# Kernel optimization log

Hardware: AMD Instinct MI355X
Metric: run time of the kernel (lower is better)

The kernel has to match this reference:

```python
import jax, jax.numpy as jnp
import numpy as np

K = 3  # number of propagation hops in SGConv


def setup_inputs() -> dict:
    key = jax.random.key(0)
    k1, k2, k3, k4 = jax.random.split(key, 4)
    N, E, F_in, F_out = 100000, 1600000, 32, 64
    x = jax.random.normal(k1, (N, F_in), dtype=jnp.float32)
    edge_index = jax.random.randint(k2, (2, E), 0, N, dtype=jnp.int64)
    # Linear(in_channels, hidden_channels) params, torch layout: W [out, in], b [out]
    lim = 1.0 / np.sqrt(F_in)
    W = jax.random.uniform(k3, (F_out, F_in), minval=-lim, maxval=lim, dtype=jnp.float32)
    b = jax.random.uniform(k4, (F_out,), minval=-lim, maxval=lim, dtype=jnp.float32)
    return {"x": x, "edge_index": edge_index, "W": W, "b": b}


def reference(x, edge_index, W, b):
    N = x.shape[0]
    # gcn_norm: add self-loops with weight 1, symmetric normalization
    loop = jnp.arange(N, dtype=edge_index.dtype)
    src = jnp.concatenate([edge_index[0], loop])  # [E+N] message sources (x_j)
    dst = jnp.concatenate([edge_index[1], loop])  # [E+N] aggregation targets
    ones = jnp.ones(src.shape[0], dtype=x.dtype)
    deg = jax.ops.segment_sum(ones, dst, num_segments=N)  # in-degree incl. self-loop
    dinv = jnp.where(deg > 0, jax.lax.rsqrt(deg), 0.0)
    norm = dinv[src] * dinv[dst]  # [E+N]
    # K hops of normalized sparse propagation: x <- \hat{A} x
    h = x
    for _ in range(K):
        h = jax.ops.segment_sum(norm[:, None] * h[src], dst, num_segments=N)
    # final linear transform
    return h @ W.T + b
```

## Files before the change

kernel.cpp:

```cpp
#include <hip/hip_runtime.h>


#define F_IN 32
#define F_OUT 64
#define SB_SHIFT 13
#define MAXSB 16
#define SUB_SHIFT 9
#define SUB (1 << SUB_SHIFT)
#define EPB1 2048
#define EPB2 4096
#define SCAP 147456
#define SUBCAP 12288
#define BPS (SCAP / EPB2)

typedef float f4 __attribute__((ext_vector_type(4)));
typedef _Float16 h4 __attribute__((ext_vector_type(4)));
typedef int i2 __attribute__((ext_vector_type(2)));

__global__ __launch_bounds__(256) void k_bin1(const int* __restrict__ ei,
                                              int* __restrict__ scur,
                                              unsigned* __restrict__ b1, int E) {
    __shared__ unsigned stage[EPB1];
    __shared__ unsigned char bidl[EPB1];
    __shared__ int hist[MAXSB], lscan[MAXSB], lbase[MAXSB], fcur[MAXSB];
    unsigned rec[EPB1 / 256];
    int      bk[EPB1 / 256];
    int tid = threadIdx.x;
    int base = blockIdx.x * EPB1;
    int cnt = E - base; if (cnt > EPB1) cnt = EPB1;

    if (tid < MAXSB) hist[tid] = 0;
    __syncthreads();
#pragma unroll
    for (int k = 0; k < EPB1 / 256; ++k) {
        int i = base + k * 256 + tid;
        bk[k] = -1;
        if (i < E) {
            unsigned s = (unsigned)ei[i];
            unsigned d = (unsigned)ei[E + i];
            int b = d >> SB_SHIFT;
            rec[k] = (s << SB_SHIFT) | (d & ((1u << SB_SHIFT) - 1));
            bk[k] = b;
            atomicAdd(&hist[b], 1);
        }
    }
    __syncthreads();
    if (tid < 64) {
        int c = (tid < MAXSB) ? hist[tid] : 0;
        int inc = c;
#pragma unroll
        for (int off = 1; off < MAXSB; off <<= 1) {
            int t = __shfl_up(inc, off);
            if (tid >= off) inc += t;
        }
        if (tid < MAXSB) {
            lscan[tid] = inc - c;
            fcur[tid] = inc - c;
            lbase[tid] = c ? atomicAdd(&scur[tid], c) : 0;
        }
    }
    __syncthreads();
#pragma unroll
    for (int k = 0; k < EPB1 / 256; ++k) {
        if (bk[k] >= 0) {
            int loc = atomicAdd(&fcur[bk[k]], 1);
            stage[loc] = rec[k];
            bidl[loc] = (unsigned char)bk[k];
        }
    }
    __syncthreads();
    for (int k = 0; k < EPB1 / 256; ++k) {
        int idx = k * 256 + tid;
        if (idx < cnt) {
            int b = bidl[idx];
            b1[(size_t)b * SCAP + lbase[b] + (idx - lscan[b])] = stage[idx];
        }
    }
}

__global__ __launch_bounds__(256) void k_bin2(const unsigned* __restrict__ b1,
                                              const int* __restrict__ scur,
                                              int* __restrict__ subcur,
                                              unsigned* __restrict__ b2) {
    int sb = blockIdx.x / BPS;
    int base = (blockIdx.x % BPS) * EPB2;
    int count = scur[sb];
    if (base >= count) return;
    int cnt = count - base; if (cnt > EPB2) cnt = EPB2;
    const unsigned* src = b1 + (size_t)sb * SCAP + base;

    __shared__ unsigned stage[EPB2];
    __shared__ int hist[16], lscan[16], lbase[16], fcur[16];
    unsigned rec[EPB2 / 256];
    int tid = threadIdx.x;
    if (tid < 16) hist[tid] = 0;
    __syncthreads();
#pragma unroll
    for (int k = 0; k < EPB2 / 256; ++k) {
        int i = k * 256 + tid;
        rec[k] = 0xFFFFFFFFu;
        if (i < cnt) {
            unsigned r = src[i];
            rec[k] = r;
            atomicAdd(&hist[(r >> SUB_SHIFT) & 15], 1);
        }
    }
    __syncthreads();
    if (tid < 64) {
        int c = (tid < 16) ? hist[tid] : 0;
        int inc = c;
#pragma unroll
        for (int off = 1; off < 16; off <<= 1) {
            int t = __shfl_up(inc, off);
            if (tid >= off) inc += t;
        }
        if (tid < 16) {
            lscan[tid] = inc - c;
            fcur[tid] = inc - c;
            lbase[tid] = c ? atomicAdd(&subcur[sb * 16 + tid], c) : 0;
        }
    }
    __syncthreads();
#pragma unroll
    for (int k = 0; k < EPB2 / 256; ++k) {
        if (rec[k] != 0xFFFFFFFFu) {
            int b = (rec[k] >> SUB_SHIFT) & 15;
            int loc = atomicAdd(&fcur[b], 1);
            stage[loc] = rec[k];
        }
    }
    __syncthreads();
    for (int k = 0; k < EPB2 / 256; ++k) {
        int idx = k * 256 + tid;
        if (idx < cnt) {
            unsigned r = stage[idx];
            int b = (r >> SUB_SHIFT) & 15;
            unsigned packed = ((r >> SB_SHIFT) << SUB_SHIFT) | (r & (SUB - 1));
            b2[(size_t)(sb * 16 + b) * SUBCAP + lbase[b] + (idx - lscan[b])] = packed;
        }
    }
}

__global__ __launch_bounds__(512) void k_fill3(const unsigned* __restrict__ b2,
                                               const int* __restrict__ subcur,
                                               float* __restrict__ dinv,
                                               i2* __restrict__ rp2,
                                               int* __restrict__ col, int N) {
    __shared__ unsigned stage[SUBCAP];
    __shared__ int h[SUB];
    __shared__ int wsum[8];
    int tid = threadIdx.x;
    int g = blockIdx.x;
    int count = subcur[g];
    int sbase = g * SUBCAP;

    h[tid] = 0;
    for (int e = tid; e < count; e += 512) stage[e] = b2[(size_t)sbase + e];
    __syncthreads();
    for (int e = tid; e < count; e += 512) atomicAdd(&h[stage[e] & (SUB - 1)], 1);
    __syncthreads();

    int deg = h[tid];
    int lane = tid & 63, wid = tid >> 6;
    int inc = deg;
#pragma unroll
    for (int off = 1; off < 64; off <<= 1) {
        int t = __shfl_up(inc, off);
        if (lane >= off) inc += t;
    }
    if (lane == 63) wsum[wid] = inc;
    __syncthreads();
    if (wid == 0) {
        int v = (lane < 8) ? wsum[lane] : 0;
#pragma unroll
        for (int off = 1; off < 8; off <<= 1) {
            int t = __shfl_up(v, off);
            if (lane >= off) v += t;
        }
        if (lane < 8) wsum[lane] = v;
    }
    __syncthreads();
    int incl = inc + (wid ? wsum[wid - 1] : 0);
    int excl = incl - deg;

    int node = (g << SUB_SHIFT) + tid;
    if (node < N) {
        dinv[node] = rsqrtf(1.0f + (float)deg);
        rp2[node] = (i2){sbase + excl, sbase + incl};
    }
    h[tid] = excl;
    __syncthreads();

    for (int e = tid; e < count; e += 512) {
        unsigned r = stage[e];
        int slot = sbase + atomicAdd(&h[r & (SUB - 1)], 1);
        col[slot] = (int)(r >> SUB_SHIFT);
    }
}

__global__ void k_prescale(const f4* __restrict__ x, const float* __restrict__ dinv,
                           h4* __restrict__ g, int N8) {
    int t = blockIdx.x * blockDim.x + threadIdx.x;
    if (t < N8) {
        f4 v = dinv[t >> 3] * x[t];
        g[t] = __builtin_convertvector(v, h4);
    }
}

__global__ __launch_bounds__(256) void k_hop_gather(const i2* __restrict__ rp2,
                                                    const int* __restrict__ col,
                                                    const float* __restrict__ dinv,
                                                    const h4* __restrict__ gin,
                                                    h4* __restrict__ gout, int N) {
    int t = blockIdx.x * blockDim.x + threadIdx.x;
    int n = t >> 3;
    if (n >= N) return;
    int q = t & 7;
    i2 r2 = rp2[n];
    int e0 = r2.x, e1 = r2.y;
    f4 a0 = __builtin_convertvector(gin[n * 8 + q], f4);
    f4 a1 = {0.f, 0.f, 0.f, 0.f};
    int e = e0;
    for (; e + 3 < e1; e += 4) {
        int s0 = col[e], s1 = col[e + 1], s2 = col[e + 2], s3 = col[e + 3];
        h4 h0 = gin[s0 * 8 + q];
        h4 h1 = gin[s1 * 8 + q];
        h4 h2 = gin[s2 * 8 + q];
        h4 h3 = gin[s3 * 8 + q];
        a0 += __builtin_convertvector(h0, f4);
        a1 += __builtin_convertvector(h1, f4);
        a0 += __builtin_convertvector(h2, f4);
        a1 += __builtin_convertvector(h3, f4);
    }
    for (; e < e1; ++e) a0 += __builtin_convertvector(gin[col[e] * 8 + q], f4);
    float di = dinv[n];
    float sc = di * di;
    f4 r = sc * (a0 + a1);
    gout[n * 8 + q] = __builtin_convertvector(r, h4);
}

__global__ __launch_bounds__(256) void k_hop3_linear(const i2* __restrict__ rp2,
                                                     const int* __restrict__ col,
                                                     const float* __restrict__ dinv,
                                                     const h4* __restrict__ gin,
                                                     const float* __restrict__ W,
                                                     const float* __restrict__ bias,
                                                     float* __restrict__ out, int N) {
    __shared__ float Wl[F_OUT][F_IN + 1];
    __shared__ float hl[32][F_IN + 1];
    int tid = threadIdx.x;
    for (int idx = tid; idx < F_OUT * F_IN; idx += 256)
        Wl[idx >> 5][idx & 31] = W[idx];

    int nl = tid >> 3;
    int q = tid & 7;
    int n = blockIdx.x * 32 + nl;
    if (n < N) {
        i2 r2 = rp2[n];
        int e0 = r2.x, e1 = r2.y;
        f4 a0 = __builtin_convertvector(gin[n * 8 + q], f4);
        f4 a1 = {0.f, 0.f, 0.f, 0.f};
        int e = e0;
        for (; e + 3 < e1; e += 4) {
            int s0 = col[e], s1 = col[e + 1], s2 = col[e + 2], s3 = col[e + 3];
            h4 h0 = gin[s0 * 8 + q];
            h4 h1 = gin[s1 * 8 + q];
            h4 h2 = gin[s2 * 8 + q];
            h4 h3 = gin[s3 * 8 + q];
            a0 += __builtin_convertvector(h0, f4);
            a1 += __builtin_convertvector(h1, f4);
            a0 += __builtin_convertvector(h2, f4);
            a1 += __builtin_convertvector(h3, f4);
        }
        for (; e < e1; ++e) a0 += __builtin_convertvector(gin[col[e] * 8 + q], f4);
        float di = dinv[n];
        f4 r = di * (a0 + a1);
        hl[nl][q * 4 + 0] = r.x;
        hl[nl][q * 4 + 1] = r.y;
        hl[nl][q * 4 + 2] = r.z;
        hl[nl][q * 4 + 3] = r.w;
    }
    __syncthreads();
    int obase = q * 8;
    if (n < N) {
        float acc[8];
#pragma unroll
        for (int j = 0; j < 8; ++j) acc[j] = bias[obase + j];
#pragma unroll
        for (int f = 0; f < F_IN; ++f) {
            float hv = hl[nl][f];
#pragma unroll
            for (int j = 0; j < 8; ++j) acc[j] += hv * Wl[obase + j][f];
        }
        float* op = out + (size_t)n * F_OUT + obase;
        f4 v0 = {acc[0], acc[1], acc[2], acc[3]};
        f4 v1 = {acc[4], acc[5], acc[6], acc[7]};
        *(f4*)op = v0;
        *(f4*)(op + 4) = v1;
    }
}

extern "C" void kernel_launch(void* const* d_in, const int* in_sizes, int n_in,
                              void* d_out, int out_size, void* d_ws, size_t ws_size,
                              hipStream_t stream) {
    const float* x  = (const float*)d_in[0];
    const int*   ei = (const int*)d_in[1];
    const float* W  = (const float*)d_in[2];
    const float* b  = (const float*)d_in[3];
    float* out = (float*)d_out;

    const int N = in_sizes[0] / F_IN;
    const int E = in_sizes[1] / 2;
    const int NSUB = (N + SUB - 1) >> SUB_SHIFT;

    int* scur   = (int*)d_ws;
    int* subcur = scur + MAXSB;
    i2*  rp2    = (i2*)(subcur + MAXSB * 16);
    float* dinv = (float*)(rp2 + N);
    unsigned* b1 = (unsigned*)(((uintptr_t)(dinv + N) + 255) & ~(uintptr_t)255);
    unsigned* b2 = b1 + (size_t)MAXSB * SCAP;
    int* col     = (int*)(b2 + (size_t)MAXSB * 16 * SUBCAP);
    _Float16* hA = (_Float16*)(((uintptr_t)(col + (size_t)MAXSB * 16 * SUBCAP) + 255)
                               & ~(uintptr_t)255);
    _Float16* hB  = hA + (size_t)N * F_IN;
    _Float16* hB2 = hB + (size_t)N * F_IN;

    const int B = 256;
    dim3 blk(B);

    hipMemsetAsync(scur, 0, (MAXSB + MAXSB * 16) * sizeof(int), stream);

    k_bin1<<<dim3((E + EPB1 - 1) / EPB1), blk, 0, stream>>>(ei, scur, b1, E);
    k_bin2<<<dim3(((N + (1 << SB_SHIFT) - 1) >> SB_SHIFT) * BPS), blk, 0, stream>>>(
        b1, scur, subcur, b2);

    k_fill3<<<dim3(NSUB), dim3(512), 0, stream>>>(b2, subcur, dinv, rp2, col, N);

    const int N8 = N * 8;
    k_prescale<<<dim3((N8 + B - 1) / B), blk, 0, stream>>>((const f4*)x, dinv, (h4*)hA, N8);

    dim3 gHop(((size_t)N * 8 + B - 1) / B);
    k_hop_gather<<<gHop, blk, 0, stream>>>(rp2, col, dinv, (const h4*)hA, (h4*)hB, N);
    k_hop_gather<<<gHop, blk, 0, stream>>>(rp2, col, dinv, (const h4*)hB, (h4*)hB2, N);

    k_hop3_linear<<<dim3((N + 31) / 32), blk, 0, stream>>>(rp2, col, dinv,
                                                           (const h4*)hB2, W, b, out, N);
}
```

Baseline: 212.3 us.

## Fuse prescale into CSR fill, use finer sub-buckets and per-wave histograms

```diff
diff --git a/kernel.cpp b/kernel.cpp
--- a/kernel.cpp
+++ b/kernel.cpp
@@ -4,13 +4,14 @@
 #define F_IN 32
 #define F_OUT 64
 #define SB_SHIFT 13
-#define MAXSB 16
-#define SUB_SHIFT 9
+#define NSB_MAX 16
+#define SUB_SHIFT 8
 #define SUB (1 << SUB_SHIFT)
+#define SPS 32
 #define EPB1 2048
 #define EPB2 4096
 #define SCAP 147456
-#define SUBCAP 12288
+#define SUBCAP 6144
 #define BPS (SCAP / EPB2)
 
 typedef float f4 __attribute__((ext_vector_type(4)));
@@ -22,14 +23,17 @@
                                               unsigned* __restrict__ b1, int E) {
     __shared__ unsigned stage[EPB1];
     __shared__ unsigned char bidl[EPB1];
-    __shared__ int hist[MAXSB], lscan[MAXSB], lbase[MAXSB], fcur[MAXSB];
+    __shared__ int h4w[4][NSB_MAX];
+    __shared__ int f4w[4][NSB_MAX];
+    __shared__ int lscanx[NSB_MAX], lbase[NSB_MAX];
     unsigned rec[EPB1 / 256];
     int      bk[EPB1 / 256];
     int tid = threadIdx.x;
+    int wv = tid >> 6;
     int base = blockIdx.x * EPB1;
     int cnt = E - base; if (cnt > EPB1) cnt = EPB1;
 
-    if (tid < MAXSB) hist[tid] = 0;
+    if (tid < 64) { h4w[tid >> 4][tid & 15] = 0; }
     __syncthreads();
 #pragma unroll
     for (int k = 0; k < EPB1 / 256; ++k) {
@@ -41,29 +45,32 @@
             int b = d >> SB_SHIFT;
             rec[k] = (s << SB_SHIFT) | (d & ((1u << SB_SHIFT) - 1));
             bk[k] = b;
-            atomicAdd(&hist[b], 1);
-        }
-    }
-    __syncthreads();
-    if (tid < 64) {
-        int c = (tid < MAXSB) ? hist[tid] : 0;
-        int inc = c;
-#pragma unroll
-        for (int off = 1; off < MAXSB; off <<= 1) {
+            atomicAdd(&h4w[wv][b], 1);
+        }
+    }
+    __syncthreads();
+    if (tid < 16) {
+        int t0 = h4w[0][tid], t1 = h4w[1][tid], t2 = h4w[2][tid], t3 = h4w[3][tid];
+        int tot = t0 + t1 + t2 + t3;
+        int inc = tot;
+#pragma unroll
+        for (int off = 1; off < 16; off <<= 1) {
             int t = __shfl_up(inc, off);
             if (tid >= off) inc += t;
         }
-        if (tid < MAXSB) {
-            lscan[tid] = inc - c;
-            fcur[tid] = inc - c;
-            lbase[tid] = c ? atomicAdd(&scur[tid], c) : 0;
-        }
+        int excl = inc - tot;
+        lscanx[tid] = excl;
+        lbase[tid] = tot ? atomicAdd(&scur[tid], tot) : 0;
+        f4w[0][tid] = excl;
+        f4w[1][tid] = excl + t0;
+        f4w[2][tid] = excl + t0 + t1;
+        f4w[3][tid] = excl + t0 + t1 + t2;
     }
     __syncthreads();
 #pragma unroll
     for (int k = 0; k < EPB1 / 256; ++k) {
         if (bk[k] >= 0) {
-            int loc = atomicAdd(&fcur[bk[k]], 1);
+            int loc = atomicAdd(&f4w[wv][bk[k]], 1);
             stage[loc] = rec[k];
             bidl[loc] = (unsigned char)bk[k];
         }
@@ -73,7 +80,7 @@
         int idx = k * 256 + tid;
         if (idx < cnt) {
             int b = bidl[idx];
-            b1[(size_t)b * SCAP + lbase[b] + (idx - lscan[b])] = stage[idx];
+            b1[(size_t)b * SCAP + lbase[b] + (idx - lscanx[b])] = stage[idx];
         }
     }
 }
@@ -90,10 +97,14 @@
     const unsigned* src = b1 + (size_t)sb * SCAP + base;
 
     __shared__ unsigned stage[EPB2];
-    __shared__ int hist[16], lscan[16], lbase[16], fcur[16];
+    __shared__ unsigned char bidl[EPB2];
+    __shared__ int h4w[4][SPS];
+    __shared__ int f4w[4][SPS];
+    __shared__ int lscanx[SPS], lbase[SPS];
     unsigned rec[EPB2 / 256];
     int tid = threadIdx.x;
-    if (tid < 16) hist[tid] = 0;
+    int wv = tid >> 6;
+    if (tid < 128) h4w[tid >> 5][tid & 31] = 0;
     __syncthreads();
 #pragma unroll
     for (int k = 0; k < EPB2 / 256; ++k) {
@@ -102,31 +113,35 @@
         if (i < cnt) {
             unsigned r = src[i];
             rec[k] = r;
-            atomicAdd(&hist[(r >> SUB_SHIFT) & 15], 1);
-        }
-    }
-    __syncthreads();
-    if (tid < 64) {
-        int c = (tid < 16) ? hist[tid] : 0;
-        int inc = c;
-#pragma unroll
-        for (int off = 1; off < 16; off <<= 1) {
+            atomicAdd(&h4w[wv][(r >> SUB_SHIFT) & (SPS - 1)], 1);
+        }
+    }
+    __syncthreads();
+    if (tid < 32) {
+        int t0 = h4w[0][tid], t1 = h4w[1][tid], t2 = h4w[2][tid], t3 = h4w[3][tid];
+        int tot = t0 + t1 + t2 + t3;
+        int inc = tot;
+#pragma unroll
+        for (int off = 1; off < 32; off <<= 1) {
             int t = __shfl_up(inc, off);
             if (tid >= off) inc += t;
         }
-        if (tid < 16) {
-            lscan[tid] = inc - c;
-            fcur[tid] = inc - c;
-            lbase[tid] = c ? atomicAdd(&subcur[sb * 16 + tid], c) : 0;
-        }
+        int excl = inc - tot;
+        lscanx[tid] = excl;
+        lbase[tid] = tot ? atomicAdd(&subcur[sb * SPS + tid], tot) : 0;
+        f4w[0][tid] = excl;
+        f4w[1][tid] = excl + t0;
+        f4w[2][tid] = excl + t0 + t1;
+        f4w[3][tid] = excl + t0 + t1 + t2;
     }
     __syncthreads();
 #pragma unroll
     for (int k = 0; k < EPB2 / 256; ++k) {
         if (rec[k] != 0xFFFFFFFFu) {
-            int b = (rec[k] >> SUB_SHIFT) & 15;
-            int loc = atomicAdd(&fcur[b], 1);
+            int b = (rec[k] >> SUB_SHIFT) & (SPS - 1);
+            int loc = atomicAdd(&f4w[wv][b], 1);
             stage[loc] = rec[k];
+            bidl[loc] = (unsigned char)b;
         }
     }
     __syncthreads();
@@ -134,30 +149,34 @@
         int idx = k * 256 + tid;
         if (idx < cnt) {
             unsigned r = stage[idx];
-            int b = (r >> SUB_SHIFT) & 15;
+            int b = bidl[idx];
             unsigned packed = ((r >> SB_SHIFT) << SUB_SHIFT) | (r & (SUB - 1));
-            b2[(size_t)(sb * 16 + b) * SUBCAP + lbase[b] + (idx - lscan[b])] = packed;
-        }
-    }
-}
-
-__global__ __launch_bounds__(512) void k_fill3(const unsigned* __restrict__ b2,
+            b2[(size_t)(sb * SPS + b) * SUBCAP + lbase[b] + (idx - lscanx[b])] = packed;
+        }
+    }
+}
+
+__global__ __launch_bounds__(256) void k_fill3(const unsigned* __restrict__ b2,
                                                const int* __restrict__ subcur,
+                                               const f4* __restrict__ x,
                                                float* __restrict__ dinv,
                                                i2* __restrict__ rp2,
-                                               int* __restrict__ col, int N) {
+                                               int* __restrict__ col,
+                                               h4* __restrict__ g0, int N) {
     __shared__ unsigned stage[SUBCAP];
     __shared__ int h[SUB];
-    __shared__ int wsum[8];
+    __shared__ float dl[SUB];
+    __shared__ int wsum[4];
     int tid = threadIdx.x;
     int g = blockIdx.x;
     int count = subcur[g];
     int sbase = g * SUBCAP;
+    int n0 = g << SUB_SHIFT;
 
     h[tid] = 0;
-    for (int e = tid; e < count; e += 512) stage[e] = b2[(size_t)sbase + e];
-    __syncthreads();
-    for (int e = tid; e < count; e += 512) atomicAdd(&h[stage[e] & (SUB - 1)], 1);
+    for (int e = tid; e < count; e += 256) stage[e] = b2[(size_t)sbase + e];
+    __syncthreads();
+    for (int e = tid; e < count; e += 256) atomicAdd(&h[stage[e] & (SUB - 1)], 1);
     __syncthreads();
 
     int deg = h[tid];
@@ -171,39 +190,41 @@
     if (lane == 63) wsum[wid] = inc;
     __syncthreads();
     if (wid == 0) {
-        int v = (lane < 8) ? wsum[lane] : 0;
-#pragma unroll
-        for (int off = 1; off < 8; off <<= 1) {
+        int v = (lane < 4) ? wsum[lane] : 0;
+#pragma unroll
+        for (int off = 1; off < 4; off <<= 1) {
             int t = __shfl_up(v, off);
             if (lane >= off) v += t;
         }
-        if (lane < 8) wsum[lane] = v;
+        if (lane < 4) wsum[lane] = v;
     }
     __syncthreads();
     int incl = inc + (wid ? wsum[wid - 1] : 0);
     int excl = incl - deg;
 
-    int node = (g << SUB_SHIFT) + tid;
+    int node = n0 + tid;
+    float di = rsqrtf(1.0f + (float)deg);
+    dl[tid] = di;
     if (node < N) {
-        dinv[node] = rsqrtf(1.0f + (float)deg);
+        dinv[node] = di;
         rp2[node] = (i2){sbase + excl, sbase + incl};
     }
     h[tid] = excl;
     __syncthreads();
 
-    for (int e = tid; e < count; e += 512) {
+    for (int e = tid; e < count; e += 256) {
         unsigned r = stage[e];
         int slot = sbase + atomicAdd(&h[r & (SUB - 1)], 1);
         col[slot] = (int)(r >> SUB_SHIFT);
     }
-}
-
-__global__ void k_prescale(const f4* __restrict__ x, const float* __restrict__ dinv,
-                           h4* __restrict__ g, int N8) {
-    int t = blockIdx.x * blockDim.x + threadIdx.x;
-    if (t < N8) {
-        f4 v = dinv[t >> 3] * x[t];
-        g[t] = __builtin_convertvector(v, h4);
+
+    for (int idx = tid; idx < SUB * 8; idx += 256) {
+        int nl = idx >> 3;
+        int gi = n0 * 8 + idx;
+        if (n0 + nl < N) {
+            f4 v = dl[nl] * x[gi];
+            g0[gi] = __builtin_convertvector(v, h4);
+        }
     }
 }
 
@@ -254,7 +275,8 @@
 
     int nl = tid >> 3;
     int q = tid & 7;
-    int n = blockIdx.x * 32 + nl;
+    int nbase = blockIdx.x * 32;
+    int n = nbase + nl;
     if (n < N) {
         i2 r2 = rp2[n];
         int e0 = r2.x, e1 = r2.y;
@@ -281,22 +303,22 @@
         hl[nl][q * 4 + 3] = r.w;
     }
     __syncthreads();
-    int obase = q * 8;
-    if (n < N) {
-        float acc[8];
-#pragma unroll
-        for (int j = 0; j < 8; ++j) acc[j] = bias[obase + j];
-#pragma unroll
-        for (int f = 0; f < F_IN; ++f) {
-            float hv = hl[nl][f];
-#pragma unroll
-            for (int j = 0; j < 8; ++j) acc[j] += hv * Wl[obase + j][f];
-        }
-        float* op = out + (size_t)n * F_OUT + obase;
-        f4 v0 = {acc[0], acc[1], acc[2], acc[3]};
-        f4 v1 = {acc[4], acc[5], acc[6], acc[7]};
-        *(f4*)op = v0;
-        *(f4*)(op + 4) = v1;
+    int o = tid & 63;
+    float wreg[F_IN];
+#pragma unroll
+    for (int f = 0; f < F_IN; ++f) wreg[f] = Wl[o][f];
+    float bv = bias[o];
+    int nchunk = tid >> 6;
+#pragma unroll
+    for (int p = 0; p < 8; ++p) {
+        int nloc = p * 4 + nchunk;
+        int nn = nbase + nloc;
+        if (nn < N) {
+            float acc = bv;
+#pragma unroll
+            for (int f = 0; f < F_IN; ++f) acc += hl[nloc][f] * wreg[f];
+            out[(size_t)nn * F_OUT + o] = acc;
+        }
     }
 }
 
@@ -311,16 +333,17 @@
 
     const int N = in_sizes[0] / F_IN;
     const int E = in_sizes[1] / 2;
+    const int NSB  = (N + (1 << SB_SHIFT) - 1) >> SB_SHIFT;
     const int NSUB = (N + SUB - 1) >> SUB_SHIFT;
 
     int* scur   = (int*)d_ws;
-    int* subcur = scur + MAXSB;
-    i2*  rp2    = (i2*)(subcur + MAXSB * 16);
+    int* subcur = scur + NSB_MAX;
+    i2*  rp2    = (i2*)(subcur + NSB_MAX * SPS);
     float* dinv = (float*)(rp2 + N);
     unsigned* b1 = (unsigned*)(((uintptr_t)(dinv + N) + 255) & ~(uintptr_t)255);
-    unsigned* b2 = b1 + (size_t)MAXSB * SCAP;
-    int* col     = (int*)(b2 + (size_t)MAXSB * 16 * SUBCAP);
-    _Float16* hA = (_Float16*)(((uintptr_t)(col + (size_t)MAXSB * 16 * SUBCAP) + 255)
+    unsigned* b2 = b1 + (size_t)NSB_MAX * SCAP;
+    int* col     = (int*)(b2 + (size_t)NSB_MAX * SPS * SUBCAP);
+    _Float16* hA = (_Float16*)(((uintptr_t)(col + (size_t)NSB_MAX * SPS * SUBCAP) + 255)
                                & ~(uintptr_t)255);
     _Float16* hB  = hA + (size_t)N * F_IN;
     _Float16* hB2 = hB + (size_t)N * F_IN;
@@ -328,16 +351,13 @@
     const int B = 256;
     dim3 blk(B);
 
-    hipMemsetAsync(scur, 0, (MAXSB + MAXSB * 16) * sizeof(int), stream);
+    hipMemsetAsync(scur, 0, (NSB_MAX + NSB_MAX * SPS) * sizeof(int), stream);
 
     k_bin1<<<dim3((E + EPB1 - 1) / EPB1), blk, 0, stream>>>(ei, scur, b1, E);
-    k_bin2<<<dim3(((N + (1 << SB_SHIFT) - 1) >> SB_SHIFT) * BPS), blk, 0, stream>>>(
-        b1, scur, subcur, b2);
-
-    k_fill3<<<dim3(NSUB), dim3(512), 0, stream>>>(b2, subcur, dinv, rp2, col, N);
-
-    const int N8 = N * 8;
-    k_prescale<<<dim3((N8 + B - 1) / B), blk, 0, stream>>>((const f4*)x, dinv, (h4*)hA, N8);
+    k_bin2<<<dim3(NSB * BPS), blk, 0, stream>>>(b1, scur, subcur, b2);
+
+    k_fill3<<<dim3(NSUB), blk, 0, stream>>>(b2, subcur, (const f4*)x,
+                                            dinv, rp2, col, (h4*)hA, N);
 
     dim3 gHop(((size_t)N * 8 + B - 1) / B);
     k_hop_gather<<<gHop, blk, 0, stream>>>(rp2, col, dinv, (const h4*)hA, (h4*)hB, N);
```

Measured after the change: 201.8 us, median of 2. 4.9% less time.
